# Optimization experiments

Hardware: AMD Instinct MI355X
Metric: run time of the kernel (lower is better)

Reference implementation:

```python
import jax, jax.numpy as jnp
import numpy as np

NUM_PATCHES = 10
SIGMA = 4.0            # size_exp_deadzone
PAD_X = 16             # padding_deadzone_size_x
PAD_Y = 16             # padding_deadzone_size_y
DEADZONE_EXP = True
HARD_CUTOUT = True     # deadzone_hard_cutout == 1
HARD_CUTOUT_SIZE = 4.0


def setup_inputs() -> dict:
    key = jax.random.key(0)
    k1, k2, k3, k4 = jax.random.split(key, 4)
    B, C, H, W = 8, 1, 256, 256
    D, KH, KW = 64, 1, 33
    inp = {
        "input": jax.random.normal(k1, (B, C, H, W), dtype=jnp.float32),
        "dictionary_filter": jax.random.normal(k2, (64, C, 33, 33), dtype=jnp.float32),
        "dictionary": jax.random.normal(k3, (64, C, 33, 33), dtype=jnp.float32),
        "dictionary_prior": jax.random.uniform(k4, (64,), dtype=jnp.float32),
    }
    return inp


def _fourier_convolution(contour, dictionary_filter):
    # contour: [B,C,H,W], dictionary_filter: [D,C,kh,kw] (kh,kw odd)
    B, C, H, W = contour.shape
    D, _, kh, kw = dictionary_filter.shape
    filt = jnp.flip(dictionary_filter, axis=(-2, -1))
    padded = jnp.zeros((D, C, H, W), dtype=contour.dtype).at[:, :, :kh, :kw].set(filt)
    padded = jnp.roll(padded, shift=(-(kh // 2), -(kw // 2)), axis=(-2, -1))
    filt_fft = jnp.fft.rfft2(padded)                 # [D,C,H,W//2+1]
    contour_fft = jnp.fft.rfft2(contour)             # [B,C,H,W//2+1]
    # [B,D,C,H,W] -> sum over channel C -> [B,D,H,W]
    conv = jnp.fft.irfft2(contour_fft[:, None] * filt_fft[None], s=(H, W)).sum(axis=2)
    return conv


def reference(input, dictionary_filter, dictionary, dictionary_prior):
    B, C, H, W = input.shape
    dt = input.dtype
    conv = _fourier_convolution(input, dictionary_filter)  # [B,D,H,W]

    use_map = jnp.ones((B, H, W), dtype=dt)
    if PAD_X > 0:
        use_map = use_map.at[:, :PAD_X, :].set(0.0).at[:, -PAD_X:, :].set(0.0)
    if PAD_Y > 0:
        use_map = use_map.at[:, :, :PAD_Y].set(0.0).at[:, :, -PAD_Y:].set(0.0)

    xs = jnp.arange(H, dtype=dt)
    ys = jnp.arange(W, dtype=dt)
    batch_idx = jnp.arange(B)

    def step(use_map, _):
        # search tensor: conv * use_map * prior  -> [B,D,H,W]
        search = conv * use_map[:, None] * dictionary_prior[None, :, None, None]
        flat = search.reshape(B, -1)
        idx = jnp.argmax(flat, axis=1)                    # [B]
        ov0 = jnp.max(flat, axis=1)                       # saliency incl. prior
        d = idx // (H * W)
        rem = idx % (H * W)
        px = rem // W
        py = rem % W
        ov1 = conv[batch_idx, d, px, py]                  # raw overlap
        # deadzone centered at (px,py)
        dx = xs[None, :] - px[:, None].astype(dt)         # [B,H]
        dy = ys[None, :] - py[:, None].astype(dt)         # [B,W]
        dist2 = dx[:, :, None] ** 2 + dy[:, None, :] ** 2  # [B,H,W]
        if DEADZONE_EXP:
            tmap = 1.0 - jnp.exp(-dist2 / (2.0 * SIGMA ** 2))
        else:
            tmap = jnp.ones_like(dist2)
        if HARD_CUTOUT:
            tmap = tmap * jnp.where(dist2 <= HARD_CUTOUT_SIZE ** 2, 0.0, 1.0)
        new_use = use_map * tmap
        new_use = new_use / jnp.max(new_use, axis=(1, 2), keepdims=True)
        pos = jnp.stack([d, px, py], axis=1)              # [B,3]
        ov = jnp.stack([ov0, ov1], axis=1)                # [B,2]
        return new_use, (pos, ov)

    _, (pos, ov) = jax.lax.scan(step, use_map, None, length=NUM_PATCHES)
    position_found = jnp.transpose(pos, (1, 0, 2))  # [B, num_patches, 3] int
    overlap_found = jnp.transpose(ov, (1, 0, 2))    # [B, num_patches, 2]
    return position_found, overlap_found
```

## Files before the change

### kernel.cpp

```cpp
#include <hip/hip_runtime.h>

typedef unsigned long long u64;
typedef unsigned int u32;
typedef unsigned short ushort_t;

using f32x16 = __attribute__((ext_vector_type(16))) float;
using f32x4  = __attribute__((ext_vector_type(4))) float;
using short8 = __attribute__((ext_vector_type(8))) short;

#define NB 8
#define NPIX 65536
#define CAND_CAP 65536
#define MARGIN 45.0f

__device__ __forceinline__ u32 fsort(float f){
  u32 u = __float_as_uint(f);
  return (u & 0x80000000u) ? ~u : (u | 0x80000000u);
}
__device__ __forceinline__ float funsort(u32 s){
  u32 u = (s & 0x80000000u) ? (s ^ 0x80000000u) : ~s;
  return __uint_as_float(u);
}
__device__ __forceinline__ u32 rneb(float f){
  u32 x = __float_as_uint(f);
  return (x + 0x7fffu + ((x >> 16) & 1u)) >> 16;
}
__device__ __forceinline__ float bf2f(u32 h){ return __uint_as_float(h << 16); }

__global__ __launch_bounds__(256) void prep_kernel(
    const float* __restrict__ filt, const float* __restrict__ prior,
    ushort_t* __restrict__ afh, ushort_t* __restrict__ acolh,
    float* __restrict__ fcorner, float* __restrict__ priorR,
    float* __restrict__ filtT4, float* __restrict__ filtC,
    u32* __restrict__ ncand, u32* __restrict__ mmax)
{
  int t = blockIdx.x * 256 + threadIdx.x;
  if (t == 0) *ncand = 0u;
  if (t < 8) mmax[t] = 0u;
  for (int i = t; i < 67584; i += 16384){
    int j = i & 7; int fidx = i >> 3; int lane = fidx & 63; int rest = fidx >> 6;
    int dt = rest & 1; int kc = (rest >> 1) & 1; int fy = rest >> 2;
    int d = dt * 32 + (lane & 31);
    int fx = 16 * kc + 8 * (lane >> 5) + j;
    afh[i] = (ushort_t)rneb(filt[d * 1089 + fy * 33 + fx]);
  }
  for (int i = t; i < 2048; i += 16384){
    int j = i & 7; int fidx = i >> 3; int lane = fidx & 63; int rest = fidx >> 6;
    int dt = rest & 1; int kc = rest >> 1;
    int d = dt * 32 + (lane & 31);
    int fy = 16 * kc + 8 * (lane >> 5) + j;
    acolh[i] = (ushort_t)rneb(filt[d * 1089 + fy * 33 + 32]);
  }
  for (int i = t; i < 2048; i += 16384){
    int reg = i & 15; int rest = i >> 4; int lane = rest & 63; int dt = rest >> 6;
    int d = dt * 32 + (reg & 3) + 8 * (reg >> 2) + 4 * (lane >> 5);
    fcorner[i] = filt[d * 1089 + 1088];
    priorR[i] = prior[d];
  }
  for (int i = t; i < 67584; i += 16384){
    int e = i & 3; int d = (i >> 2) & 63; int q = (i >> 8) & 7; int fy = i >> 11;
    filtT4[i] = filt[d * 1089 + fy * 33 + 4 * q + e];
  }
  for (int i = t; i < 2112; i += 16384){
    int d = i & 63; int fy = i >> 6;
    filtC[i] = filt[d * 1089 + fy * 33 + 32];
  }
}

__device__ __forceinline__ u32 funnel(u32 hi, u32 lo, int sh){
  return (u32)((((u64)hi << 32) | (u64)lo) >> sh);
}
template<int J>
__device__ __forceinline__ short8 extractf(uint4 P0, uint4 P1, int sh){
  u32 W[8] = {P0.x, P0.y, P0.z, P0.w, P1.x, P1.y, P1.z, P1.w};
  uint4 t;
  t.x = funnel(W[J + 1], W[J + 0], sh);
  t.y = funnel(W[J + 2], W[J + 1], sh);
  t.z = funnel(W[J + 3], W[J + 2], sh);
  t.w = funnel(W[J + 4], W[J + 3], sh);
  return __builtin_bit_cast(short8, t);
}
__device__ __forceinline__ f32x16 zero16(){
  f32x16 v;
  #pragma unroll
  for (int i = 0; i < 16; ++i) v[i] = 0.f;
  return v;
}

template<int J>
__device__ __forceinline__ void conv_body(
    const char* ldsc, const ushort_t* lds16, int w, int l, int tX,
    const short8* __restrict__ afh8, const short8* __restrict__ acol8,
    const f32x4* __restrict__ fcp, const f32x4* __restrict__ prp,
    u64* __restrict__ pb, int sh)
{
  const int c = l & 31, h = l >> 5;
  const int y0 = w;
  int cob0[2], cob1[2];
  #pragma unroll
  for (int kc = 0; kc < 2; ++kc){
    int yp = (y0 + 8 * c + 16 * kc + 8 * h - 16) & 255;
    int b0 = yp >> 3, b1 = (b0 + 1) & 31;
    cob0[kc] = b0 * 16; cob1[kc] = b1 * 16;
  }
  const int cc = (y0 + 8 * c + 16) & 255;

#define LA(DST, FY)                                                           \
  { _Pragma("unroll")                                                         \
    for (int kc = 0; kc < 2; ++kc)                                            \
      _Pragma("unroll")                                                       \
      for (int dt = 0; dt < 2; ++dt)                                          \
        DST[kc][dt] = afh8[(((FY) * 2 + kc) * 2 + dt) * 64 + l]; }

#define LW(S, ROWI)                                                           \
  { const char* rb_ = ldsc + (ROWI) * 512;                                    \
    s##S##k0p0 = *(const uint4*)(rb_ + cob0[0]);                              \
    s##S##k0p1 = *(const uint4*)(rb_ + cob1[0]);                              \
    s##S##k1p0 = *(const uint4*)(rb_ + cob0[1]);                              \
    s##S##k1p1 = *(const uint4*)(rb_ + cob1[1]); }

#define CPH(SA, SB, ACUR, ANXT, FYP, DOPF)                                    \
  { if (DOPF){ LA(ANXT, FYP) }                                                \
    short8 b0k0 = extractf<J>(s##SA##k0p0, s##SA##k0p1, sh);                  \
    short8 b0k1 = extractf<J>(s##SA##k1p0, s##SA##k1p1, sh);                  \
    short8 b1k0 = extractf<J>(s##SB##k0p0, s##SB##k0p1, sh);                  \
    short8 b1k1 = extractf<J>(s##SB##k1p0, s##SB##k1p1, sh);                  \
    acc[0][0] = __builtin_amdgcn_mfma_f32_32x32x16_bf16(ACUR[0][0], b0k0, acc[0][0], 0, 0, 0); \
    acc[0][0] = __builtin_amdgcn_mfma_f32_32x32x16_bf16(ACUR[1][0], b0k1, acc[0][0], 0, 0, 0); \
    acc[0][1] = __builtin_amdgcn_mfma_f32_32x32x16_bf16(ACUR[0][1], b0k0, acc[0][1], 0, 0, 0); \
    acc[0][1] = __builtin_amdgcn_mfma_f32_32x32x16_bf16(ACUR[1][1], b0k1, acc[0][1], 0, 0, 0); \
    acc[1][0] = __builtin_amdgcn_mfma_f32_32x32x16_bf16(ACUR[0][0], b1k0, acc[1][0], 0, 0, 0); \
    acc[1][0] = __builtin_amdgcn_mfma_f32_32x32x16_bf16(ACUR[1][0], b1k1, acc[1][0], 0, 0, 0); \
    acc[1][1] = __builtin_amdgcn_mfma_f32_32x32x16_bf16(ACUR[0][1], b1k0, acc[1][1], 0, 0, 0); \
    acc[1][1] = __builtin_amdgcn_mfma_f32_32x32x16_bf16(ACUR[1][1], b1k1, acc[1][1], 0, 0, 0); }

  for (int g0 = 0; g0 < 2; ++g0){
    const int r0 = g0 * 2;
    f32x16 acc[2][2];
    #pragma unroll
    for (int nr = 0; nr < 2; ++nr)
      #pragma unroll
      for (int dt = 0; dt < 2; ++dt) acc[nr][dt] = zero16();

    uint4 s0k0p0, s0k0p1, s0k1p0, s0k1p1;
    uint4 s1k0p0, s1k0p1, s1k1p0, s1k1p1;
    short8 aA[2][2], aB[2][2];

    LW(0, r0)
    LW(1, r0 + 1)
    LA(aA, 0)

    #pragma unroll 1
    for (int fy2 = 0; fy2 < 32; fy2 += 2){
      CPH(0, 1, aA, aB, fy2 + 1, true)
      LW(0, r0 + fy2 + 2)
      CPH(1, 0, aB, aA, fy2 + 2, true)
      LW(1, r0 + fy2 + 3)
    }
    CPH(0, 1, aA, aB, 0, false)

    #pragma unroll
    for (int nr = 0; nr < 2; ++nr){
      #pragma unroll
      for (int kc = 0; kc < 2; ++kc){
        int base = (r0 + nr + 16 * kc + 8 * h) * 512 + cc * 2;
        u32 v0 = *(const ushort_t*)(ldsc + base + 0 * 512);
        u32 v1 = *(const ushort_t*)(ldsc + base + 1 * 512);
        u32 v2 = *(const ushort_t*)(ldsc + base + 2 * 512);
        u32 v3 = *(const ushort_t*)(ldsc + base + 3 * 512);
        u32 v4 = *(const ushort_t*)(ldsc + base + 4 * 512);
        u32 v5 = *(const ushort_t*)(ldsc + base + 5 * 512);
        u32 v6 = *(const ushort_t*)(ldsc + base + 6 * 512);
        u32 v7 = *(const ushort_t*)(ldsc + base + 7 * 512);
        uint4 t;
        t.x = v0 | (v1 << 16); t.y = v2 | (v3 << 16);
        t.z = v4 | (v5 << 16); t.w = v6 | (v7 << 16);
        short8 Bc = __builtin_bit_cast(short8, t);
        #pragma unroll
        for (int dt = 0; dt < 2; ++dt)
          acc[nr][dt] = __builtin_amdgcn_mfma_f32_32x32x16_bf16(
              acol8[(kc * 2 + dt) * 64 + l], Bc, acc[nr][dt], 0, 0, 0);
      }
    }

    #pragma unroll
    for (int nr = 0; nr < 2; ++nr){
      float cv = bf2f((u32)lds16[(r0 + nr + 32) * 256 + cc]);
      float bv = -3e38f; int bd = 0;
      #pragma unroll
      for (int dt = 0; dt < 2; ++dt){
        #pragma unroll
        for (int q = 0; q < 4; ++q){
          f32x4 fc4 = fcp[(dt * 64 + l) * 4 + q];
          f32x4 pr4 = prp[(dt * 64 + l) * 4 + q];
          #pragma unroll
          for (int e = 0; e < 4; ++e){
            int reg = q * 4 + e;
            float s = (acc[nr][dt][reg] + fc4[e] * cv) * pr4[e];
            int d = dt * 32 + e + 8 * q + 4 * h;
            if (s > bv || (s == bv && d < bd)){ bv = s; bd = d; }
          }
        }
      }
      int x = tX + r0 + nr;
      int y = y0 + 8 * c;
      u64 key = ((u64)fsort(bv) << 32) | (u64)(63 - bd);
      u64 other = __shfl_xor(key, 32);
      if (other > key) key = other;
      if (h == 0) pb[(x << 8) | y] = key;
    }
  }
#undef CPH
#undef LW
#undef LA
}

__global__ __launch_bounds__(512) void conv_mfma(
    const float* __restrict__ input,
    const ushort_t* __restrict__ afh, const ushort_t* __restrict__ acolh,
    const float* __restrict__ fcorner, const float* __restrict__ priorR,
    u64* __restrict__ packed)
{
  __shared__ ushort_t lds[9216];
  const int bS = blockIdx.x;
  const int b  = blockIdx.y;
  const int tX = bS * 4;
  const int tid = threadIdx.x;

  const float* inb = input + b * NPIX;
  for (int k = tid; k < 1152; k += 512){
    int r = k >> 5, u = k & 31;
    int gx = (tX - 16 + r) & 255;
    const float* src = inb + (gx << 8) + (u << 3);
    float4 v1 = *(const float4*)(src);
    float4 v2 = *(const float4*)(src + 4);
    uint4 t;
    t.x = rneb(v1.x) | (rneb(v1.y) << 16);
    t.y = rneb(v1.z) | (rneb(v1.w) << 16);
    t.z = rneb(v2.x) | (rneb(v2.y) << 16);
    t.w = rneb(v2.z) | (rneb(v2.w) << 16);
    *(uint4*)((char*)lds + r * 512 + u * 16) = t;
  }
  __syncthreads();

  const int w = tid >> 6, l = tid & 63;
  u64* pb = packed + b * NPIX;
  const int sh = 16 * (w & 1);
  const char* ldsc = (const char*)lds;
  const short8* afh8 = (const short8*)afh;
  const short8* acol8 = (const short8*)acolh;
  const f32x4* fcp = (const f32x4*)fcorner;
  const f32x4* prp = (const f32x4*)priorR;

  switch ((w >> 1) & 3){
    case 0: conv_body<0>(ldsc, lds, w, l, tX, afh8, acol8, fcp, prp, pb, sh); break;
    case 1: conv_body<1>(ldsc, lds, w, l, tX, afh8, acol8, fcp, prp, pb, sh); break;
    case 2: conv_body<2>(ldsc, lds, w, l, tX, afh8, acol8, fcp, prp, pb, sh); break;
    default: conv_body<3>(ldsc, lds, w, l, tX, afh8, acol8, fcp, prp, pb, sh); break;
  }
}

__global__ __launch_bounds__(256) void bmax_kernel(const u64* __restrict__ packed,
                                                   u32* __restrict__ mmax){
  const int b = blockIdx.y, blk = blockIdx.x, tid = threadIdx.x;
  const u32* ph = (const u32*)(packed + b * NPIX);
  u32 m = 0;
  for (int k = tid; k < 2048; k += 256) m = max(m, ph[2 * (blk * 2048 + k) + 1]);
  __shared__ u32 red[256];
  red[tid] = m; __syncthreads();
  for (int s = 128; s > 0; s >>= 1){
    if (tid < s) red[tid] = max(red[tid], red[tid + s]);
    __syncthreads();
  }
  if (tid == 0) atomicMax(&mmax[b], red[0]);
}

__global__ __launch_bounds__(256) void collect_kernel(const u64* __restrict__ packed,
    const u32* __restrict__ mmax, u32* __restrict__ ncand, u32* __restrict__ cand){
  const int b = blockIdx.y, blk = blockIdx.x, tid = threadIdx.x;
  float M = funsort(mmax[b]);
  u32 tu = fsort(M - MARGIN);
  const u32* ph = (const u32*)(packed + b * NPIX);
  for (int k = tid; k < 2048; k += 256){
    int p = blk * 2048 + k;
    u32 v = ph[2 * p + 1];
    if (v >= tu){
      u32 slot = atomicAdd(ncand, 1u);
      if (slot < CAND_CAP) cand[slot] = ((u32)b << 16) | (u32)p;
    }
  }
}

__global__ __launch_bounds__(256) void rerank_kernel(
    const float* __restrict__ input, const float* __restrict__ filtT4,
    const float* __restrict__ filtC, const float* __restrict__ prior,
    const u32* __restrict__ ncand, const u32* __restrict__ cand,
    u64* __restrict__ packed)
{
  const int lane = threadIdx.x & 63;
  const int wv = threadIdx.x >> 6;
  int n = (int)min(*ncand, (u32)CAND_CAP);
  float pv = prior[lane];
  for (int i = blockIdx.x * 4 + wv; i < n; i += 4096){
    u32 v = cand[i];
    int b = v >> 16, p = v & 0xffff;
    int px = p >> 8, py = p & 255;
    if (px < 16 || px >= 240 || py < 16 || py >= 240) continue;
    int yc = py - 16;
    float s0 = 0.f, s1 = 0.f, s2 = 0.f, s3 = 0.f;
    for (int fy = 0; fy < 33; ++fy){
      const float* ir = input + b * NPIX + ((px + fy - 16) << 8) + yc;
      const float* ft = filtT4 + fy * 2048 + lane * 4;
      #pragma unroll
      for (int q = 0; q < 8; ++q){
        const float4 fv = *(const float4*)(ft + q * 256);
        s0 = fmaf(fv.x, ir[4*q+0], s0);
        s1 = fmaf(fv.y, ir[4*q+1], s1);
        s2 = fmaf(fv.z, ir[4*q+2], s2);
        s3 = fmaf(fv.w, ir[4*q+3], s3);
      }
      s0 = fmaf(filtC[fy * 64 + lane], ir[32], s0);
    }
    float s = (s0 + s2) + (s1 + s3);
    u64 key = ((u64)fsort(s * pv) << 32) | (u64)(63 - lane);
    #pragma unroll
    for (int off = 32; off; off >>= 1){
      u64 o = __shfl_down(key, off);
      if (o > key) key = o;
    }
    if (lane == 0) packed[b * NPIX + p] = key;
  }
}

__global__ __launch_bounds__(1024) void greedy_kernel(
    const u64* __restrict__ packed, const float* __restrict__ prior,
    float* __restrict__ out)
{
  const int b = blockIdx.x;
  const int tid = threadIdx.x;
  const u64* pb = packed + b * NPIX;
  const u32* ph = (const u32*)pb;

  const int x = tid >> 2;
  const int ybase = (tid & 3) << 6;
  const int pbase = (x << 8) + ybase;

  float s[64];
  const bool rowin = (x >= 16 && x < 240);
  #pragma unroll
  for (int i = 0; i < 64; ++i){
    int y = ybase + i;
    float bvv = funsort(ph[2 * (pbase + i) + 1]);
    s[i] = (rowin && y >= 16 && y < 240) ? bvv : 0.0f;
  }
  float tm = -3e38f; int tp = pbase;
  #pragma unroll
  for (int i = 0; i < 64; ++i){
    if (s[i] > tm){ tm = s[i]; tp = pbase + i; }
  }

  __shared__ u64 warr[16];
  __shared__ int spx, spy;
  if (tid == 0){ spx = -100000; spy = -100000; }
  __syncthreads();

  for (int t = 0; t < 10; ++t){
    const int px = spx, py = spy;
    if (px >= 0){
      int dxr = x - px;
      if (dxr >= -24 && dxr <= 24){
        int lo = py - 24 - ybase;
        int hi = py + 24 - ybase;
        if (lo < 64 && hi >= 0){
          float dx2 = (float)(dxr * dxr);
          tm = -3e38f; tp = pbase;
          #pragma unroll
          for (int i = 0; i < 64; ++i){
            if (i >= lo && i <= hi){
              float dy = (float)(ybase + i - py);
              float d2 = dx2 + dy * dy;
              float tmap = 1.f - __expf(d2 * -0.03125f);
              if (d2 <= 16.f) tmap = 0.f;
              s[i] *= tmap;
            }
            if (s[i] > tm){ tm = s[i]; tp = pbase + i; }
          }
        }
      }
    }
    u64 key = ((u64)fsort(tm) << 32) | (u64)(0xFFFFu ^ (u32)tp);
    #pragma unroll
    for (int off = 32; off; off >>= 1){
      u64 o = __shfl_down(key, off);
      if (o > key) key = o;
    }
    if ((tid & 63) == 0) warr[tid >> 6] = key;
    __syncthreads();
    if (tid < 64){
      u64 k2 = (tid < 16) ? warr[tid] : 0ull;
      #pragma unroll
      for (int off = 8; off; off >>= 1){
        u64 o = __shfl_down(k2, off);
        if (o > k2) k2 = o;
      }
      if (tid == 0){
        int id = 0xFFFF ^ (int)(k2 & 0xFFFFull);
        float v = funsort((u32)(k2 >> 32));
        u64 pk = pb[id];
        int d = 63 - (int)(pk & 63ull);
        float bvv = funsort((u32)(pk >> 32));
        int xx = id >> 8, yy = id & 255;
        out[b * 30 + t * 3 + 0] = (float)d;
        out[b * 30 + t * 3 + 1] = (float)xx;
        out[b * 30 + t * 3 + 2] = (float)yy;
        out[240 + b * 20 + t * 2 + 0] = v;
        out[240 + b * 20 + t * 2 + 1] = bvv / prior[d];
        spx = xx; spy = yy;
      }
    }
    __syncthreads();
  }
}

extern "C" void kernel_launch(void* const* d_in, const int* in_sizes, int n_in,
                              void* d_out, int out_size, void* d_ws, size_t ws_size,
                              hipStream_t stream)
{
  const float* input = (const float*)d_in[0];
  const float* filt  = (const float*)d_in[1];
  const float* prior = (const float*)d_in[3];
  float* out = (float*)d_out;

  char* ws = (char*)d_ws;
  u64*      packed  = (u64*)(ws);
  u32*      ncand   = (u32*)  (ws + 4194304);
  u32*      mmax    = (u32*)  (ws + 4194368);
  ushort_t* afh     = (ushort_t*)(ws + 4194432);
  ushort_t* acolh   = (ushort_t*)(ws + 4329600);
  float*    fcorner = (float*)(ws + 4333696);
  float*    priorR  = (float*)(ws + 4341888);
  u32*      cand    = (u32*)  (ws + 4350080);
  float*    filtT4  = (float*)(ws + 4612224);
  float*    filtC   = (float*)(ws + 4882560);

  prep_kernel<<<64, 256, 0, stream>>>(filt, prior, afh, acolh, fcorner, priorR,
                                      filtT4, filtC, ncand, mmax);
  conv_mfma<<<dim3(64, NB), 512, 0, stream>>>(input, afh, acolh, fcorner, priorR, packed);
  bmax_kernel<<<dim3(32, NB), 256, 0, stream>>>(packed, mmax);
  collect_kernel<<<dim3(32, NB), 256, 0, stream>>>(packed, mmax, ncand, cand);
  rerank_kernel<<<1024, 256, 0, stream>>>(input, filtT4, filtC, prior, ncand, cand, packed);
  greedy_kernel<<<NB, 1024, 0, stream>>>(packed, prior, out);
}
```

Before: 215.8 us.

## Fuse batch-max into conv kernel and merge collect with rerank via ballot

The conv kernel now computes the per-batch maximum score with wave shuffles, a shared-memory atomic and one global atomicMax per block, so the separate bmax pass over packed is gone. The collect and rerank kernels are merged: each wave scans 64 pixels, ballots those above the margin threshold and reranks them in place. This drops the global candidate counter, the candidate list and two launches. The greedy kernel also loads two packed entries per 16-byte read. The cost is that rerank work is now spread unevenly across waves by pixel chunk rather than balanced over a compacted list.

```diff
diff --git a/kernel.cpp b/kernel.cpp
--- a/kernel.cpp
+++ b/kernel.cpp
@@ -10,7 +10,6 @@
 
 #define NB 8
 #define NPIX 65536
-#define CAND_CAP 65536
 #define MARGIN 45.0f
 
 __device__ __forceinline__ u32 fsort(float f){
@@ -32,10 +31,9 @@
     ushort_t* __restrict__ afh, ushort_t* __restrict__ acolh,
     float* __restrict__ fcorner, float* __restrict__ priorR,
     float* __restrict__ filtT4, float* __restrict__ filtC,
-    u32* __restrict__ ncand, u32* __restrict__ mmax)
+    u32* __restrict__ mmax)
 {
   int t = blockIdx.x * 256 + threadIdx.x;
-  if (t == 0) *ncand = 0u;
   if (t < 8) mmax[t] = 0u;
   for (int i = t; i < 67584; i += 16384){
     int j = i & 7; int fidx = i >> 3; int lane = fidx & 63; int rest = fidx >> 6;
@@ -92,7 +90,7 @@
     const char* ldsc, const ushort_t* lds16, int w, int l, int tX,
     const short8* __restrict__ afh8, const short8* __restrict__ acol8,
     const f32x4* __restrict__ fcp, const f32x4* __restrict__ prp,
-    u64* __restrict__ pb, int sh)
+    u64* __restrict__ pb, u32* bm, int sh)
 {
   const int c = l & 31, h = l >> 5;
   const int y0 = w;
@@ -183,6 +181,7 @@
       }
     }
 
+    u32 km32 = 0;
     #pragma unroll
     for (int nr = 0; nr < 2; ++nr){
       float cv = bf2f((u32)lds16[(r0 + nr + 32) * 256 + cc]);
@@ -208,7 +207,15 @@
       u64 other = __shfl_xor(key, 32);
       if (other > key) key = other;
       if (h == 0) pb[(x << 8) | y] = key;
-    }
+      u32 kv = (u32)(key >> 32);
+      if (kv > km32) km32 = kv;
+    }
+    #pragma unroll
+    for (int off = 32; off; off >>= 1){
+      u32 o = __shfl_down(km32, off);
+      if (o > km32) km32 = o;
+    }
+    if (l == 0) atomicMax(bm, km32);
   }
 #undef CPH
 #undef LW
@@ -219,13 +226,15 @@
     const float* __restrict__ input,
     const ushort_t* __restrict__ afh, const ushort_t* __restrict__ acolh,
     const float* __restrict__ fcorner, const float* __restrict__ priorR,
-    u64* __restrict__ packed)
+    u64* __restrict__ packed, u32* __restrict__ mmax)
 {
   __shared__ ushort_t lds[9216];
+  __shared__ u32 bm;
   const int bS = blockIdx.x;
   const int b  = blockIdx.y;
   const int tX = bS * 4;
   const int tid = threadIdx.x;
+  if (tid == 0) bm = 0u;
 
   const float* inb = input + b * NPIX;
   for (int k = tid; k < 1152; k += 512){
@@ -253,60 +262,39 @@
   const f32x4* prp = (const f32x4*)priorR;
 
   switch ((w >> 1) & 3){
-    case 0: conv_body<0>(ldsc, lds, w, l, tX, afh8, acol8, fcp, prp, pb, sh); break;
-    case 1: conv_body<1>(ldsc, lds, w, l, tX, afh8, acol8, fcp, prp, pb, sh); break;
-    case 2: conv_body<2>(ldsc, lds, w, l, tX, afh8, acol8, fcp, prp, pb, sh); break;
-    default: conv_body<3>(ldsc, lds, w, l, tX, afh8, acol8, fcp, prp, pb, sh); break;
-  }
-}
-
-__global__ __launch_bounds__(256) void bmax_kernel(const u64* __restrict__ packed,
-                                                   u32* __restrict__ mmax){
-  const int b = blockIdx.y, blk = blockIdx.x, tid = threadIdx.x;
+    case 0: conv_body<0>(ldsc, lds, w, l, tX, afh8, acol8, fcp, prp, pb, &bm, sh); break;
+    case 1: conv_body<1>(ldsc, lds, w, l, tX, afh8, acol8, fcp, prp, pb, &bm, sh); break;
+    case 2: conv_body<2>(ldsc, lds, w, l, tX, afh8, acol8, fcp, prp, pb, &bm, sh); break;
+    default: conv_body<3>(ldsc, lds, w, l, tX, afh8, acol8, fcp, prp, pb, &bm, sh); break;
+  }
+  __syncthreads();
+  if (tid == 0) atomicMax(&mmax[b], bm);
+}
+
+__global__ __launch_bounds__(256) void collect_rerank(
+    const float* __restrict__ input, const float* __restrict__ filtT4,
+    const float* __restrict__ filtC, const float* __restrict__ prior,
+    const u32* __restrict__ mmax, u64* __restrict__ packed)
+{
+  const int lane = threadIdx.x & 63;
+  const int g = blockIdx.x * 4 + (threadIdx.x >> 6);
+  const int b = g >> 10;
+  const int chunk = (g & 1023) << 6;
   const u32* ph = (const u32*)(packed + b * NPIX);
-  u32 m = 0;
-  for (int k = tid; k < 2048; k += 256) m = max(m, ph[2 * (blk * 2048 + k) + 1]);
-  __shared__ u32 red[256];
-  red[tid] = m; __syncthreads();
-  for (int s = 128; s > 0; s >>= 1){
-    if (tid < s) red[tid] = max(red[tid], red[tid + s]);
-    __syncthreads();
-  }
-  if (tid == 0) atomicMax(&mmax[b], red[0]);
-}
-
-__global__ __launch_bounds__(256) void collect_kernel(const u64* __restrict__ packed,
-    const u32* __restrict__ mmax, u32* __restrict__ ncand, u32* __restrict__ cand){
-  const int b = blockIdx.y, blk = blockIdx.x, tid = threadIdx.x;
+  const int px = chunk >> 8;
   float M = funsort(mmax[b]);
   u32 tu = fsort(M - MARGIN);
-  const u32* ph = (const u32*)(packed + b * NPIX);
-  for (int k = tid; k < 2048; k += 256){
-    int p = blk * 2048 + k;
-    u32 v = ph[2 * p + 1];
-    if (v >= tu){
-      u32 slot = atomicAdd(ncand, 1u);
-      if (slot < CAND_CAP) cand[slot] = ((u32)b << 16) | (u32)p;
-    }
-  }
-}
-
-__global__ __launch_bounds__(256) void rerank_kernel(
-    const float* __restrict__ input, const float* __restrict__ filtT4,
-    const float* __restrict__ filtC, const float* __restrict__ prior,
-    const u32* __restrict__ ncand, const u32* __restrict__ cand,
-    u64* __restrict__ packed)
-{
-  const int lane = threadIdx.x & 63;
-  const int wv = threadIdx.x >> 6;
-  int n = (int)min(*ncand, (u32)CAND_CAP);
+  int p = chunk + lane;
+  int py = p & 255;
+  bool qual = (ph[2 * p + 1] >= tu) &&
+              (px >= 16) && (px < 240) && (py >= 16) && (py < 240);
+  u64 mask = __ballot(qual);
   float pv = prior[lane];
-  for (int i = blockIdx.x * 4 + wv; i < n; i += 4096){
-    u32 v = cand[i];
-    int b = v >> 16, p = v & 0xffff;
-    int px = p >> 8, py = p & 255;
-    if (px < 16 || px >= 240 || py < 16 || py >= 240) continue;
-    int yc = py - 16;
+  while (mask){
+    int bit = __ffsll((unsigned long long)mask) - 1;
+    mask &= mask - 1;
+    int pc = chunk + bit;
+    int yc = (pc & 255) - 16;
     float s0 = 0.f, s1 = 0.f, s2 = 0.f, s3 = 0.f;
     for (int fy = 0; fy < 33; ++fy){
       const float* ir = input + b * NPIX + ((px + fy - 16) << 8) + yc;
@@ -328,7 +316,7 @@
       u64 o = __shfl_down(key, off);
       if (o > key) key = o;
     }
-    if (lane == 0) packed[b * NPIX + p] = key;
+    if (lane == 0) packed[b * NPIX + pc] = key;
   }
 }
 
@@ -339,7 +327,6 @@
   const int b = blockIdx.x;
   const int tid = threadIdx.x;
   const u64* pb = packed + b * NPIX;
-  const u32* ph = (const u32*)pb;
 
   const int x = tid >> 2;
   const int ybase = (tid & 3) << 6;
@@ -348,10 +335,11 @@
   float s[64];
   const bool rowin = (x >= 16 && x < 240);
   #pragma unroll
-  for (int i = 0; i < 64; ++i){
-    int y = ybase + i;
-    float bvv = funsort(ph[2 * (pbase + i) + 1]);
-    s[i] = (rowin && y >= 16 && y < 240) ? bvv : 0.0f;
+  for (int i2 = 0; i2 < 32; ++i2){
+    uint4 two = *(const uint4*)(pb + pbase + 2 * i2);
+    int y = ybase + 2 * i2;
+    s[2*i2+0] = (rowin && y+0 >= 16 && y+0 < 240) ? funsort(two.y) : 0.0f;
+    s[2*i2+1] = (rowin && y+1 >= 16 && y+1 < 240) ? funsort(two.w) : 0.0f;
   }
   float tm = -3e38f; int tp = pbase;
   #pragma unroll
@@ -433,21 +421,18 @@
 
   char* ws = (char*)d_ws;
   u64*      packed  = (u64*)(ws);
-  u32*      ncand   = (u32*)  (ws + 4194304);
-  u32*      mmax    = (u32*)  (ws + 4194368);
-  ushort_t* afh     = (ushort_t*)(ws + 4194432);
-  ushort_t* acolh   = (ushort_t*)(ws + 4329600);
-  float*    fcorner = (float*)(ws + 4333696);
-  float*    priorR  = (float*)(ws + 4341888);
-  u32*      cand    = (u32*)  (ws + 4350080);
-  float*    filtT4  = (float*)(ws + 4612224);
-  float*    filtC   = (float*)(ws + 4882560);
+  u32*      mmax    = (u32*)  (ws + 4194304);
+  ushort_t* afh     = (ushort_t*)(ws + 4194368);
+  ushort_t* acolh   = (ushort_t*)(ws + 4329536);
+  float*    fcorner = (float*)(ws + 4333632);
+  float*    priorR  = (float*)(ws + 4341824);
+  float*    filtT4  = (float*)(ws + 4350016);
+  float*    filtC   = (float*)(ws + 4620352);
 
   prep_kernel<<<64, 256, 0, stream>>>(filt, prior, afh, acolh, fcorner, priorR,
-                                      filtT4, filtC, ncand, mmax);
-  conv_mfma<<<dim3(64, NB), 512, 0, stream>>>(input, afh, acolh, fcorner, priorR, packed);
-  bmax_kernel<<<dim3(32, NB), 256, 0, stream>>>(packed, mmax);
-  collect_kernel<<<dim3(32, NB), 256, 0, stream>>>(packed, mmax, ncand, cand);
-  rerank_kernel<<<1024, 256, 0, stream>>>(input, filtT4, filtC, prior, ncand, cand, packed);
+                                      filtT4, filtC, mmax);
+  conv_mfma<<<dim3(64, NB), 512, 0, stream>>>(input, afh, acolh, fcorner, priorR,
+                                              packed, mmax);
+  collect_rerank<<<2048, 256, 0, stream>>>(input, filtT4, filtC, prior, mmax, packed);
   greedy_kernel<<<NB, 1024, 0, stream>>>(packed, prior, out);
 }
```

Result: no change. 217.6 us (+0.9%).

## Derive rerank candidate threshold from a preliminary greedy pass instead of global max

Applied to the files above, without the earlier changes.

Runs the greedy selection once on the approximate bf16 scores to find the 10th picked value per batch. Candidates are then collected relative to that value minus a slack, with border pixels filtered at collection time instead of in rerank. This replaces the bmax reduction and is meant to shrink the candidate set sent to the exact fp32 rerank. The cost is an extra greedy pass, plus a correctness risk if the smaller slack misses true winners. The greedy kernel's loads are also vectorised to read two packed entries at a time.

```diff
diff --git a/kernel.cpp b/kernel.cpp
--- a/kernel.cpp
+++ b/kernel.cpp
@@ -11,7 +11,7 @@
 #define NB 8
 #define NPIX 65536
 #define CAND_CAP 65536
-#define MARGIN 45.0f
+#define SLACK 12.0f
 
 __device__ __forceinline__ u32 fsort(float f){
   u32 u = __float_as_uint(f);
@@ -32,11 +32,10 @@
     ushort_t* __restrict__ afh, ushort_t* __restrict__ acolh,
     float* __restrict__ fcorner, float* __restrict__ priorR,
     float* __restrict__ filtT4, float* __restrict__ filtC,
-    u32* __restrict__ ncand, u32* __restrict__ mmax)
+    u32* __restrict__ ncand)
 {
   int t = blockIdx.x * 256 + threadIdx.x;
   if (t == 0) *ncand = 0u;
-  if (t < 8) mmax[t] = 0u;
   for (int i = t; i < 67584; i += 16384){
     int j = i & 7; int fidx = i >> 3; int lane = fidx & 63; int rest = fidx >> 6;
     int dt = rest & 1; int kc = (rest >> 1) & 1; int fy = rest >> 2;
@@ -260,31 +259,16 @@
   }
 }
 
-__global__ __launch_bounds__(256) void bmax_kernel(const u64* __restrict__ packed,
-                                                   u32* __restrict__ mmax){
+__global__ __launch_bounds__(256) void collect_kernel(const u64* __restrict__ packed,
+    const float* __restrict__ tmin, u32* __restrict__ ncand, u32* __restrict__ cand){
   const int b = blockIdx.y, blk = blockIdx.x, tid = threadIdx.x;
-  const u32* ph = (const u32*)(packed + b * NPIX);
-  u32 m = 0;
-  for (int k = tid; k < 2048; k += 256) m = max(m, ph[2 * (blk * 2048 + k) + 1]);
-  __shared__ u32 red[256];
-  red[tid] = m; __syncthreads();
-  for (int s = 128; s > 0; s >>= 1){
-    if (tid < s) red[tid] = max(red[tid], red[tid + s]);
-    __syncthreads();
-  }
-  if (tid == 0) atomicMax(&mmax[b], red[0]);
-}
-
-__global__ __launch_bounds__(256) void collect_kernel(const u64* __restrict__ packed,
-    const u32* __restrict__ mmax, u32* __restrict__ ncand, u32* __restrict__ cand){
-  const int b = blockIdx.y, blk = blockIdx.x, tid = threadIdx.x;
-  float M = funsort(mmax[b]);
-  u32 tu = fsort(M - MARGIN);
+  u32 tu = fsort(tmin[b] - SLACK);
   const u32* ph = (const u32*)(packed + b * NPIX);
   for (int k = tid; k < 2048; k += 256){
     int p = blk * 2048 + k;
+    int px = p >> 8, py = p & 255;
     u32 v = ph[2 * p + 1];
-    if (v >= tu){
+    if (v >= tu && px >= 16 && px < 240 && py >= 16 && py < 240){
       u32 slot = atomicAdd(ncand, 1u);
       if (slot < CAND_CAP) cand[slot] = ((u32)b << 16) | (u32)p;
     }
@@ -304,9 +288,8 @@
   for (int i = blockIdx.x * 4 + wv; i < n; i += 4096){
     u32 v = cand[i];
     int b = v >> 16, p = v & 0xffff;
-    int px = p >> 8, py = p & 255;
-    if (px < 16 || px >= 240 || py < 16 || py >= 240) continue;
-    int yc = py - 16;
+    int px = p >> 8;
+    int yc = (p & 255) - 16;
     float s0 = 0.f, s1 = 0.f, s2 = 0.f, s3 = 0.f;
     for (int fy = 0; fy < 33; ++fy){
       const float* ir = input + b * NPIX + ((px + fy - 16) << 8) + yc;
@@ -334,12 +317,11 @@
 
 __global__ __launch_bounds__(1024) void greedy_kernel(
     const u64* __restrict__ packed, const float* __restrict__ prior,
-    float* __restrict__ out)
+    float* __restrict__ out, float* __restrict__ tmin)
 {
   const int b = blockIdx.x;
   const int tid = threadIdx.x;
   const u64* pb = packed + b * NPIX;
-  const u32* ph = (const u32*)pb;
 
   const int x = tid >> 2;
   const int ybase = (tid & 3) << 6;
@@ -348,10 +330,11 @@
   float s[64];
   const bool rowin = (x >= 16 && x < 240);
   #pragma unroll
-  for (int i = 0; i < 64; ++i){
-    int y = ybase + i;
-    float bvv = funsort(ph[2 * (pbase + i) + 1]);
-    s[i] = (rowin && y >= 16 && y < 240) ? bvv : 0.0f;
+  for (int i2 = 0; i2 < 32; ++i2){
+    uint4 two = *(const uint4*)(pb + pbase + 2 * i2);
+    int y = ybase + 2 * i2;
+    s[2*i2+0] = (rowin && y+0 >= 16 && y+0 < 240) ? funsort(two.y) : 0.0f;
+    s[2*i2+1] = (rowin && y+1 >= 16 && y+1 < 240) ? funsort(two.w) : 0.0f;
   }
   float tm = -3e38f; int tp = pbase;
   #pragma unroll
@@ -416,6 +399,7 @@
         out[240 + b * 20 + t * 2 + 0] = v;
         out[240 + b * 20 + t * 2 + 1] = bvv / prior[d];
         spx = xx; spy = yy;
+        if (t == 9) tmin[b] = v;
       }
     }
     __syncthreads();
@@ -434,7 +418,7 @@
   char* ws = (char*)d_ws;
   u64*      packed  = (u64*)(ws);
   u32*      ncand   = (u32*)  (ws + 4194304);
-  u32*      mmax    = (u32*)  (ws + 4194368);
+  float*    tmin    = (float*)(ws + 4194368);
   ushort_t* afh     = (ushort_t*)(ws + 4194432);
   ushort_t* acolh   = (ushort_t*)(ws + 4329600);
   float*    fcorner = (float*)(ws + 4333696);
@@ -444,10 +428,10 @@
   float*    filtC   = (float*)(ws + 4882560);
 
   prep_kernel<<<64, 256, 0, stream>>>(filt, prior, afh, acolh, fcorner, priorR,
-                                      filtT4, filtC, ncand, mmax);
+                                      filtT4, filtC, ncand);
   conv_mfma<<<dim3(64, NB), 512, 0, stream>>>(input, afh, acolh, fcorner, priorR, packed);
-  bmax_kernel<<<dim3(32, NB), 256, 0, stream>>>(packed, mmax);
-  collect_kernel<<<dim3(32, NB), 256, 0, stream>>>(packed, mmax, ncand, cand);
+  greedy_kernel<<<NB, 1024, 0, stream>>>(packed, prior, out, tmin);
+  collect_kernel<<<dim3(32, NB), 256, 0, stream>>>(packed, tmin, ncand, cand);
   rerank_kernel<<<1024, 256, 0, stream>>>(input, filtT4, filtC, prior, ncand, cand, packed);
-  greedy_kernel<<<NB, 1024, 0, stream>>>(packed, prior, out);
-}
+  greedy_kernel<<<NB, 1024, 0, stream>>>(packed, prior, out, tmin);
+}
```

Result: slower. 263.0 us (+21.9%).

## Run greedy selection on sparse per-batch candidate list with certified dense fallback

Applied to the files above, without the earlier changes.

Candidate collection becomes per-batch, and the interior-border filter moves into the collect step so rerank no longer visits border points. Rerank launches a 2D grid with one row of blocks per batch. The greedy stage now runs its 10 iterations only over the collected candidates, held in registers at 8 per thread, instead of all 65536 pixels. It falls back to the full dense scan when the candidate list overflowed or the 10th pick falls below a certification threshold. A small transpose kernel is added to coalesce the filter reads in prep, which adds a launch plus a possible second greedy pass in the fallback case.

```diff
diff --git a/kernel.cpp b/kernel.cpp
--- a/kernel.cpp
+++ b/kernel.cpp
@@ -10,8 +10,9 @@
 
 #define NB 8
 #define NPIX 65536
-#define CAND_CAP 65536
-#define MARGIN 45.0f
+#define CAP1 8192
+#define BAND 44.0f
+#define CERT 43.0f
 
 __device__ __forceinline__ u32 fsort(float f){
   u32 u = __float_as_uint(f);
@@ -27,16 +28,31 @@
 }
 __device__ __forceinline__ float bf2f(u32 h){ return __uint_as_float(h << 16); }
 
+__global__ __launch_bounds__(256) void transpose_kernel(
+    const float* __restrict__ filt, float* __restrict__ filtT,
+    u32* __restrict__ ncand, u32* __restrict__ mmax)
+{
+  __shared__ float T[64][65];
+  const int b = blockIdx.x;
+  const int e0 = b * 64;
+  const int ecnt = min(64, 1089 - e0);
+  const int w = threadIdx.x >> 6, l = threadIdx.x & 63;
+  if (b == 0 && threadIdx.x < 8){ ncand[threadIdx.x] = 0u; mmax[threadIdx.x] = 0u; }
+  for (int d = w; d < 64; d += 4)
+    if (l < ecnt) T[d][l] = filt[d * 1089 + e0 + l];
+  __syncthreads();
+  for (int r = w; r < ecnt; r += 4)
+    filtT[(e0 + r) * 64 + l] = T[l][r];
+}
+
 __global__ __launch_bounds__(256) void prep_kernel(
-    const float* __restrict__ filt, const float* __restrict__ prior,
+    const float* __restrict__ filt, const float* __restrict__ filtT,
+    const float* __restrict__ prior,
     ushort_t* __restrict__ afh, ushort_t* __restrict__ acolh,
     float* __restrict__ fcorner, float* __restrict__ priorR,
-    float* __restrict__ filtT4, float* __restrict__ filtC,
-    u32* __restrict__ ncand, u32* __restrict__ mmax)
+    float* __restrict__ filtT4, float* __restrict__ filtC)
 {
   int t = blockIdx.x * 256 + threadIdx.x;
-  if (t == 0) *ncand = 0u;
-  if (t < 8) mmax[t] = 0u;
   for (int i = t; i < 67584; i += 16384){
     int j = i & 7; int fidx = i >> 3; int lane = fidx & 63; int rest = fidx >> 6;
     int dt = rest & 1; int kc = (rest >> 1) & 1; int fy = rest >> 2;
@@ -59,11 +75,11 @@
   }
   for (int i = t; i < 67584; i += 16384){
     int e = i & 3; int d = (i >> 2) & 63; int q = (i >> 8) & 7; int fy = i >> 11;
-    filtT4[i] = filt[d * 1089 + fy * 33 + 4 * q + e];
+    filtT4[i] = filtT[(fy * 33 + 4 * q + e) * 64 + d];
   }
   for (int i = t; i < 2112; i += 16384){
     int d = i & 63; int fy = i >> 6;
-    filtC[i] = filt[d * 1089 + fy * 33 + 32];
+    filtC[i] = filtT[(fy * 33 + 32) * 64 + d];
   }
 }
 
@@ -278,15 +294,15 @@
 __global__ __launch_bounds__(256) void collect_kernel(const u64* __restrict__ packed,
     const u32* __restrict__ mmax, u32* __restrict__ ncand, u32* __restrict__ cand){
   const int b = blockIdx.y, blk = blockIdx.x, tid = threadIdx.x;
-  float M = funsort(mmax[b]);
-  u32 tu = fsort(M - MARGIN);
+  u32 tu = fsort(funsort(mmax[b]) - BAND);
   const u32* ph = (const u32*)(packed + b * NPIX);
   for (int k = tid; k < 2048; k += 256){
     int p = blk * 2048 + k;
+    int px = p >> 8, py = p & 255;
     u32 v = ph[2 * p + 1];
-    if (v >= tu){
-      u32 slot = atomicAdd(ncand, 1u);
-      if (slot < CAND_CAP) cand[slot] = ((u32)b << 16) | (u32)p;
+    if (v >= tu && px >= 16 && px < 240 && py >= 16 && py < 240){
+      u32 slot = atomicAdd(&ncand[b], 1u);
+      if (slot < CAP1) cand[b * CAP1 + slot] = (u32)p;
     }
   }
 }
@@ -298,15 +314,14 @@
     u64* __restrict__ packed)
 {
   const int lane = threadIdx.x & 63;
-  const int wv = threadIdx.x >> 6;
-  int n = (int)min(*ncand, (u32)CAND_CAP);
+  const int b = blockIdx.y;
+  const int ws = blockIdx.x * 4 + (threadIdx.x >> 6);
+  int n = (int)min(ncand[b], (u32)CAP1);
   float pv = prior[lane];
-  for (int i = blockIdx.x * 4 + wv; i < n; i += 4096){
-    u32 v = cand[i];
-    int b = v >> 16, p = v & 0xffff;
-    int px = p >> 8, py = p & 255;
-    if (px < 16 || px >= 240 || py < 16 || py >= 240) continue;
-    int yc = py - 16;
+  for (int i = ws; i < n; i += 512){
+    int p = (int)cand[b * CAP1 + i];
+    int px = p >> 8;
+    int yc = (p & 255) - 16;
     float s0 = 0.f, s1 = 0.f, s2 = 0.f, s3 = 0.f;
     for (int fy = 0; fy < 33; ++fy){
       const float* ir = input + b * NPIX + ((px + fy - 16) << 8) + yc;
@@ -332,63 +347,50 @@
   }
 }
 
-__global__ __launch_bounds__(1024) void greedy_kernel(
+__global__ __launch_bounds__(1024) void greedy_sl(
     const u64* __restrict__ packed, const float* __restrict__ prior,
-    float* __restrict__ out)
+    const u32* __restrict__ ncand, const u32* __restrict__ cand,
+    const u32* __restrict__ mmax, float* __restrict__ out)
 {
   const int b = blockIdx.x;
   const int tid = threadIdx.x;
   const u64* pb = packed + b * NPIX;
-  const u32* ph = (const u32*)pb;
-
-  const int x = tid >> 2;
-  const int ybase = (tid & 3) << 6;
-  const int pbase = (x << 8) + ybase;
-
-  float s[64];
-  const bool rowin = (x >= 16 && x < 240);
+  const int n = (int)min(ncand[b], (u32)CAP1);
+
+  int cp[8]; float cv[8];
   #pragma unroll
-  for (int i = 0; i < 64; ++i){
-    int y = ybase + i;
-    float bvv = funsort(ph[2 * (pbase + i) + 1]);
-    s[i] = (rowin && y >= 16 && y < 240) ? bvv : 0.0f;
-  }
-  float tm = -3e38f; int tp = pbase;
-  #pragma unroll
-  for (int i = 0; i < 64; ++i){
-    if (s[i] > tm){ tm = s[i]; tp = pbase + i; }
+  for (int k = 0; k < 8; ++k){
+    int idx = tid + k * 1024;
+    if (idx < n){ cp[k] = (int)cand[b * CAP1 + idx]; cv[k] = funsort((u32)(pb[cp[k]] >> 32)); }
+    else        { cp[k] = 0; cv[k] = -3e38f; }
   }
 
   __shared__ u64 warr[16];
-  __shared__ int spx, spy;
+  __shared__ int spx, spy, okf;
+  __shared__ float v10s;
   if (tid == 0){ spx = -100000; spy = -100000; }
   __syncthreads();
 
   for (int t = 0; t < 10; ++t){
     const int px = spx, py = spy;
     if (px >= 0){
-      int dxr = x - px;
-      if (dxr >= -24 && dxr <= 24){
-        int lo = py - 24 - ybase;
-        int hi = py + 24 - ybase;
-        if (lo < 64 && hi >= 0){
-          float dx2 = (float)(dxr * dxr);
-          tm = -3e38f; tp = pbase;
-          #pragma unroll
-          for (int i = 0; i < 64; ++i){
-            if (i >= lo && i <= hi){
-              float dy = (float)(ybase + i - py);
-              float d2 = dx2 + dy * dy;
-              float tmap = 1.f - __expf(d2 * -0.03125f);
-              if (d2 <= 16.f) tmap = 0.f;
-              s[i] *= tmap;
-            }
-            if (s[i] > tm){ tm = s[i]; tp = pbase + i; }
-          }
+      #pragma unroll
+      for (int k = 0; k < 8; ++k){
+        if (tid + k * 1024 < n){
+          float dx = (float)((cp[k] >> 8) - px), dy = (float)((cp[k] & 255) - py);
+          float d2 = dx * dx + dy * dy;
+          float tmap = 1.f - __expf(d2 * -0.03125f);
+          if (d2 <= 16.f) tmap = 0.f;
+          cv[k] *= tmap;
         }
       }
     }
-    u64 key = ((u64)fsort(tm) << 32) | (u64)(0xFFFFu ^ (u32)tp);
+    u64 key = 0ull;
+    #pragma unroll
+    for (int k = 0; k < 8; ++k){
+      u64 kk = ((u64)fsort(cv[k]) << 32) | (u64)(0xFFFFu ^ (u32)cp[k]);
+      if (kk > key) key = kk;
+    }
     #pragma unroll
     for (int off = 32; off; off >>= 1){
       u64 o = __shfl_down(key, off);
@@ -416,9 +418,93 @@
         out[240 + b * 20 + t * 2 + 0] = v;
         out[240 + b * 20 + t * 2 + 1] = bvv / prior[d];
         spx = xx; spy = yy;
+        if (t == 9) v10s = v;
       }
     }
     __syncthreads();
+  }
+
+  if (tid == 0)
+    okf = (ncand[b] <= (u32)CAP1 && v10s >= funsort(mmax[b]) - CERT) ? 1 : 0;
+  __syncthreads();
+  if (okf) return;
+
+  {
+    const int x = tid >> 2;
+    const int ybase = (tid & 3) << 6;
+    const int pbase = (x << 8) + ybase;
+    float s[64];
+    const bool rowin = (x >= 16 && x < 240);
+    #pragma unroll
+    for (int i2 = 0; i2 < 32; ++i2){
+      uint4 two = *(const uint4*)(pb + pbase + 2 * i2);
+      int y = ybase + 2 * i2;
+      s[2*i2+0] = (rowin && y+0 >= 16 && y+0 < 240) ? funsort(two.y) : 0.0f;
+      s[2*i2+1] = (rowin && y+1 >= 16 && y+1 < 240) ? funsort(two.w) : 0.0f;
+    }
+    float tm = -3e38f; int tp = pbase;
+    #pragma unroll
+    for (int i = 0; i < 64; ++i){
+      if (s[i] > tm){ tm = s[i]; tp = pbase + i; }
+    }
+    if (tid == 0){ spx = -100000; spy = -100000; }
+    __syncthreads();
+    for (int t = 0; t < 10; ++t){
+      const int px = spx, py = spy;
+      if (px >= 0){
+        int dxr = x - px;
+        if (dxr >= -24 && dxr <= 24){
+          int lo = py - 24 - ybase;
+          int hi = py + 24 - ybase;
+          if (lo < 64 && hi >= 0){
+            float dx2 = (float)(dxr * dxr);
+            tm = -3e38f; tp = pbase;
+            #pragma unroll
+            for (int i = 0; i < 64; ++i){
+              if (i >= lo && i <= hi){
+                float dy = (float)(ybase + i - py);
+                float d2 = dx2 + dy * dy;
+                float tmap = 1.f - __expf(d2 * -0.03125f);
+                if (d2 <= 16.f) tmap = 0.f;
+                s[i] *= tmap;
+              }
+              if (s[i] > tm){ tm = s[i]; tp = pbase + i; }
+            }
+          }
+        }
+      }
+      u64 key = ((u64)fsort(tm) << 32) | (u64)(0xFFFFu ^ (u32)tp);
+      #pragma unroll
+      for (int off = 32; off; off >>= 1){
+        u64 o = __shfl_down(key, off);
+        if (o > key) key = o;
+      }
+      if ((tid & 63) == 0) warr[tid >> 6] = key;
+      __syncthreads();
+      if (tid < 64){
+        u64 k2 = (tid < 16) ? warr[tid] : 0ull;
+        #pragma unroll
+        for (int off = 8; off; off >>= 1){
+          u64 o = __shfl_down(k2, off);
+          if (o > k2) k2 = o;
+        }
+        if (tid == 0){
+          int id = 0xFFFF ^ (int)(k2 & 0xFFFFull);
+          float v = funsort((u32)(k2 >> 32));
+          u64 pk = pb[id];
+          int d = 63 - (int)(pk & 63ull);
+          float bvv = funsort((u32)(pk >> 32));
+          int xx = id >> 8, yy = id & 255;
+          out[b * 30 + t * 3 + 0] = (float)d;
+          out[b * 30 + t * 3 + 1] = (float)xx;
+          out[b * 30 + t * 3 + 2] = (float)yy;
+          out[240 + b * 20 + t * 2 + 0] = v;
+          out[240 + b * 20 + t * 2 + 1] = bvv / prior[d];
+          spx = xx; spy = yy;
+        }
+      }
+      __syncthreads();
+    }
   }
 }
 
@@ -442,12 +528,15 @@
   u32*      cand    = (u32*)  (ws + 4350080);
   float*    filtT4  = (float*)(ws + 4612224);
   float*    filtC   = (float*)(ws + 4882560);
-
-  prep_kernel<<<64, 256, 0, stream>>>(filt, prior, afh, acolh, fcorner, priorR,
-                                      filtT4, filtC, ncand, mmax);
+  float*    filtT   = (float*)(ws + 4891008);
+
+  transpose_kernel<<<18, 256, 0, stream>>>(filt, filtT, ncand, mmax);
+  prep_kernel<<<64, 256, 0, stream>>>(filt, filtT, prior, afh, acolh,
+                                      fcorner, priorR, filtT4, filtC);
   conv_mfma<<<dim3(64, NB), 512, 0, stream>>>(input, afh, acolh, fcorner, priorR, packed);
   bmax_kernel<<<dim3(32, NB), 256, 0, stream>>>(packed, mmax);
   collect_kernel<<<dim3(32, NB), 256, 0, stream>>>(packed, mmax, ncand, cand);
-  rerank_kernel<<<1024, 256, 0, stream>>>(input, filtT4, filtC, prior, ncand, cand, packed);
-  greedy_kernel<<<NB, 1024, 0, stream>>>(packed, prior, out);
-}
+  rerank_kernel<<<dim3(128, NB), 256, 0, stream>>>(input, filtT4, filtC, prior,
+                                                   ncand, cand, packed);
+  greedy_sl<<<NB, 1024, 0, stream>>>(packed, prior, ncand, cand, mmax, out);
+}
```

New measurement: 250.9 us. 16.3% more time.
